# Optimization experiments

Hardware: AMD Instinct MI355X
Metric: run time of the kernel (lower is better)

Reference implementation:

```python
import jax, jax.numpy as jnp
from jax import lax
import numpy as np

B, T = 256, 512
CHAR_SIZE, CHAR_DIM, HIDDEN = 10000, 50, 256
HALF = HIDDEN // 2  # per-direction hidden size


def _lstm_dir(x, Wih, Whh, bih, bhh, reverse):
    # x: [B,T,D]; Wih: [4H,D]; Whh: [4H,H]; gate order i,f,g,o (PyTorch)
    Bsz = x.shape[0]
    H = Whh.shape[1]
    xg = jnp.einsum('btd,gd->btg', x, Wih) + bih + bhh  # precompute input gates [B,T,4H]
    def step(carry, gt):
        h, c = carry
        g = gt + h @ Whh.T
        i, f, gg, o = jnp.split(g, 4, axis=-1)
        c = jax.nn.sigmoid(f) * c + jax.nn.sigmoid(i) * jnp.tanh(gg)
        h = jax.nn.sigmoid(o) * jnp.tanh(c)
        return (h, c), h
    init = (jnp.zeros((Bsz, H), x.dtype), jnp.zeros((Bsz, H), x.dtype))
    _, hs = lax.scan(step, init, jnp.swapaxes(xg, 0, 1), reverse=reverse)
    return jnp.swapaxes(hs, 0, 1)  # [B,T,H]


def setup_inputs() -> dict:
    key = jax.random.key(0)
    ks = jax.random.split(key, 10)
    scale = np.sqrt(3.0 / CHAR_DIM)
    inp = {
        'user_text_idx': jax.random.randint(ks[0], (B, T), 0, CHAR_SIZE),
        'masks': jnp.ones((B, T), jnp.float32),
        'emb': jax.random.uniform(ks[1], (CHAR_SIZE, CHAR_DIM), jnp.float32, -scale, scale),
        'Wih_f': jax.random.normal(ks[2], (4 * HALF, CHAR_DIM), jnp.float32) * 0.08,
        'Whh_f': jax.random.normal(ks[3], (4 * HALF, HALF), jnp.float32) * 0.08,
        'bih_f': jnp.zeros((4 * HALF,), jnp.float32),
        'bhh_f': jnp.zeros((4 * HALF,), jnp.float32),
        'Wih_b': jax.random.normal(ks[4], (4 * HALF, CHAR_DIM), jnp.float32) * 0.08,
        'Whh_b': jax.random.normal(ks[5], (4 * HALF, HALF), jnp.float32) * 0.08,
        'bih_b': jnp.zeros((4 * HALF,), jnp.float32),
        'bhh_b': jnp.zeros((4 * HALF,), jnp.float32),
    }
    return inp


def reference(user_text_idx, masks, emb, Wih_f, Whh_f, bih_f, bhh_f, Wih_b, Whh_b, bih_b, bhh_b):
    x = emb[user_text_idx]                                  # [B,T,D] embedding lookup
    h_f = _lstm_dir(x, Wih_f, Whh_f, bih_f, bhh_f, False)   # forward direction
    h_b = _lstm_dir(x, Wih_b, Whh_b, bih_b, bhh_b, True)    # backward direction
    out = jnp.concatenate([h_f, h_b], axis=-1)              # [B,T,HIDDEN]
    out = out - (1.0 - masks[..., None]) * 1e8              # mask pad positions
    return jnp.max(out, axis=-2)                            # masked max-pool -> [B,HIDDEN]
```

## Files before the change

### kernel.cpp

```cpp
#include <hip/hip_runtime.h>
#include <hip/hip_fp16.h>


#define TT 512
#define CH 2

typedef _Float16 f16;
typedef _Float16 f16x8 __attribute__((ext_vector_type(8)));
typedef float f32x4 __attribute__((ext_vector_type(4)));
typedef unsigned int u32;
typedef unsigned short u16;

static __device__ __forceinline__ u32 packh2(float lo, float hi) {
    union { struct { f16 x, y; } h; u32 u; } cv;
    cv.h.x = (f16)lo; cv.h.y = (f16)hi;
    return cv.u;
}
static __device__ __forceinline__ float unpk_lo(u32 u) {
    union { u32 u; struct { f16 x, y; } h; } cv; cv.u = u;
    return (float)cv.h.x;
}
static __device__ __forceinline__ float unpk_hi(u32 u) {
    union { u32 u; struct { f16 x, y; } h; } cv; cv.u = u;
    return (float)cv.h.y;
}
static __device__ __forceinline__ float fexp(float x) {
    return __builtin_amdgcn_exp2f(x * 1.44269504088896341f);
}
static __device__ __forceinline__ float frcp(float x) {
    return __builtin_amdgcn_rcpf(x);
}
static __device__ __forceinline__ float sigf(float x) {
    return frcp(1.f + fexp(-x));
}
static __device__ __forceinline__ float xor8(float x) {
    union { float f; int i; } c; c.f = x;
    c.i = __builtin_amdgcn_mov_dpp(c.i, 0x128, 0xF, 0xF, false);
    return c.f;
}
static __device__ __forceinline__ float sel4(f32x4 v, int q) {
    return (q & 2) ? ((q & 1) ? v[3] : v[2]) : ((q & 1) ? v[1] : v[0]);
}

__global__ __attribute__((amdgpu_flat_work_group_size(1024, 1024),
                          amdgpu_num_vgpr(128)))
void bilstm_gsplit_kernel(const int* __restrict__ idx,
                          const float* __restrict__ masks,
                          const float* __restrict__ emb,
                          const float* __restrict__ Wih_f, const float* __restrict__ Whh_f,
                          const float* __restrict__ bih_f, const float* __restrict__ bhh_f,
                          const float* __restrict__ Wih_b, const float* __restrict__ Whh_b,
                          const float* __restrict__ bih_b, const float* __restrict__ bhh_b,
                          float* __restrict__ out)
{
    __shared__ __align__(16) unsigned char Hbuf[2][6 * 1024];
    __shared__ u16 idx16[CH * TT];
    __shared__ u32 mbits[TT];
    __shared__ u32 exch[CH * 128];

    const int tid  = threadIdx.x;
    const int lane = tid & 63;
    const int wv   = tid >> 6;
    const int half = wv >> 3;
    const int wvh  = wv & 7;
    const int l15  = lane & 15;
    const int c4   = lane >> 4;
    const int d    = blockIdx.x & 1;
    const int g    = blockIdx.x >> 1;
    const int b0   = g * CH;
    const int rev  = d;

    const int chain = l15 & 1;
    const int q     = (l15 >> 1) & 3;
    const int role  = l15 >> 3;

    const float* Wih = d ? Wih_b : Wih_f;
    const float* Whh = d ? Whh_b : Whh_f;
    const float* bih = d ? bih_b : bih_f;
    const float* bhh = d ? bhh_b : bhh_f;

    for (int i = tid; i < CH * TT; i += 1024) {
        const int m = i >> 9, t = i & 511;
        idx16[i] = (u16)idx[(b0 + m) * TT + t];
    }
    if (tid < TT) {
        u32 mb = 0;
        for (int m = 0; m < CH; ++m)
            mb |= (masks[(b0 + m) * TT + tid] != 0.f ? 1u : 0u) << m;
        mbits[tid] = mb;
    }
    for (int i = tid; i < 2 * 6 * 1024 / 4; i += 1024)
        ((u32*)Hbuf)[i] = 0u;

    const int tb0 = half * 256 + wvh * 16;
    const int tb1 = tb0 + 128;
    f16x8 w[6][2];
    f32x4 bias4[2];
#pragma unroll
    for (int tt = 0; tt < 2; ++tt) {
        const int n = (tt ? tb1 : tb0) + l15;
        {
            const int nb_ = (tt ? tb1 : tb0) + c4 * 4;
            const float4 bi = *(const float4*)(bih + nb_);
            const float4 bh = *(const float4*)(bhh + nb_);
            bias4[tt][0] = bi.x + bh.x; bias4[tt][1] = bi.y + bh.y;
            bias4[tt][2] = bi.z + bh.z; bias4[tt][3] = bi.w + bh.w;
        }
#pragma unroll
        for (int jj = 0; jj < 4; ++jj) {
            const float2 e = *(const float2*)(Wih + n * 50 + c4 * 8 + jj * 2);
            w[0][tt][2 * jj]     = (f16)e.x;
            w[0][tt][2 * jj + 1] = (f16)e.y;
        }
#pragma unroll
        for (int j = 0; j < 8; ++j) {
            const int k = 32 + c4 * 8 + j;
            float v = 0.f;
            if (k < 50) v = Wih[n * 50 + k];
            w[1][tt][j] = (f16)v;
        }
#pragma unroll
        for (int kt = 2; kt < 6; ++kt) {
            const int kh = (kt - 2) * 32 + c4 * 8;
            const float4 e0 = *(const float4*)(Whh + n * 128 + kh);
            const float4 e1 = *(const float4*)(Whh + n * 128 + kh + 4);
            w[kt][tt][0] = (f16)e0.x; w[kt][tt][1] = (f16)e0.y;
            w[kt][tt][2] = (f16)e0.z; w[kt][tt][3] = (f16)e0.w;
            w[kt][tt][4] = (f16)e1.x; w[kt][tt][5] = (f16)e1.y;
            w[kt][tt][6] = (f16)e1.z; w[kt][tt][7] = (f16)e1.w;
        }
    }

    __syncthreads();

    if (tid < 400) {
        const int pm = tid / 25, ps = tid % 25;
        const int t0  = rev ? (TT - 1) : 0;
        const int row = idx16[(pm & 1) * TT + t0];
        const float2 e = *(const float2*)(emb + row * 50 + ps * 2);
        const int k0 = 2 * ps;
        const int kt = k0 >> 5, c4k = (k0 >> 3) & 3, j = k0 & 7;
        *(u32*)(&Hbuf[0][(kt << 10) + ((c4k * 16 + pm) << 4) + (j << 1)]) =
            packh2(e.x, e.y);
    }
    __syncthreads();

    float cst = 0.f, rm = -3e38f;

    const int hd     = wvh * 16 + c4 * 4 + q;
    const int k0h    = 64 + hd;
    const int wb_kt  = k0h >> 5;
    const int wb_c4k = (k0h >> 3) & 3;
    const int wb_j   = k0h & 7;
    const int wb_off = (wb_kt << 10) + ((wb_c4k * 16 + chain) << 4) + (wb_j << 1)
                     + role * 128;
    const int ex     = chain * 128 + hd;

    const int  tid2  = tid - 512;
    const bool pfthr = (tid2 >= 0) && (tid2 < 400);
    const int  pm2   = pfthr ? (tid2 / 25) : 0;
    const int  ps2   = pfthr ? (tid2 % 25) : 0;

    for (int s = 0; s < TT; ++s) {
        const int cur = s & 1;
        const int t   = rev ? (TT - 1 - s) : s;

        float2 e;
        int pk0 = 0;
        const bool pf = pfthr && (s + 1 < TT);
        if (pf) {
            const int t1  = rev ? (TT - 2 - s) : (s + 1);
            const int row = idx16[(pm2 & 1) * TT + t1];
            e = *(const float2*)(emb + row * 50 + ps2 * 2);
            pk0 = 2 * ps2;
        }

        const unsigned char* hb = &Hbuf[cur][0];
        f32x4 a0 = bias4[0], a1 = bias4[1];
#pragma unroll
        for (int kt = 0; kt < 6; ++kt) {
            const f16x8 bf = *(const f16x8*)(hb + (kt << 10) + (lane << 4));
            a0 = __builtin_amdgcn_mfma_f32_16x16x32_f16(w[kt][0], bf, a0, 0, 0, 0);
            a1 = __builtin_amdgcn_mfma_f32_16x16x32_f16(w[kt][1], bf, a1, 0, 0, 0);
        }
        const float v0 = sel4(a0, q);
        const float v1 = sel4(a1, q);

        const bool rB = (role != 0);
        const float a_in = rB ? v1 : (half ? (v0 + v0) : v0);
        const float sraw = sigf(a_in);
        const float sval = (half && !rB) ? (2.f * sraw - 1.f) : sraw;
        const float sx   = xor8(sval);

        if (half) {
            const float tg = rB ? sx : sval;
            const float so = rB ? sval : sx;
            if (!rB) exch[ex] = packh2(tg, so);
        }
        const float si = rB ? sx : sval;
        const float sf = rB ? sval : sx;

        __syncthreads();

        unsigned char* nb = &Hbuf[cur ^ 1][0];
        if (!half) {
            const u32 ts = exch[ex];
            const float tg = unpk_lo(ts);
            const float so = unpk_hi(ts);
            const float cc = sf * cst + si * tg;
            cst = cc;
            const float th = 2.f * sigf(cc + cc) - 1.f;
            const float hh = so * th;
            const float pen = ((mbits[t] >> chain) & 1u) ? 0.f : 1e8f;
            rm = fmaxf(rm, hh - pen);
            const u32 pkv = packh2(hh, hh);
            *(u16*)(nb + wb_off)      = (u16)pkv;
            *(u16*)(nb + wb_off + 32) = (u16)pkv;
            *(u16*)(nb + wb_off + 64) = (u16)pkv;
            *(u16*)(nb + wb_off + 96) = (u16)pkv;
        } else if (pf) {
            const int kt = pk0 >> 5, c4k = (pk0 >> 3) & 3, j = pk0 & 7;
            *(u32*)(nb + (kt << 10) + ((c4k * 16 + pm2) << 4) + (j << 1)) =
                packh2(e.x, e.y);
        }
        __syncthreads();
    }

    if (!half && !(l15 >> 3)) {
        out[(b0 + chain) * 256 + d * 128 + hd] = rm;
    }
}

extern "C" void kernel_launch(void* const* d_in, const int* in_sizes, int n_in,
                              void* d_out, int out_size, void* d_ws, size_t ws_size,
                              hipStream_t stream) {
    const int*   idx   = (const int*)d_in[0];
    const float* masks = (const float*)d_in[1];
    const float* emb   = (const float*)d_in[2];
    const float* Wih_f = (const float*)d_in[3];
    const float* Whh_f = (const float*)d_in[4];
    const float* bih_f = (const float*)d_in[5];
    const float* bhh_f = (const float*)d_in[6];
    const float* Wih_b = (const float*)d_in[7];
    const float* Whh_b = (const float*)d_in[8];
    const float* bih_b = (const float*)d_in[9];
    const float* bhh_b = (const float*)d_in[10];
    float* out = (float*)d_out;

    bilstm_gsplit_kernel<<<dim3(256), dim3(1024), 0, stream>>>(
        idx, masks, emb,
        Wih_f, Whh_f, bih_f, bhh_f,
        Wih_b, Whh_b, bih_b, bhh_b,
        out);
}
```

Baseline: 436.7 us.

## Compact per-step hidden/input LDS buffer and broadcast B operand reads

Replaces the padded 6KB-per-buffer MFMA B-operand layout with a compact [chain][192] f16 vector per batch chain, so each lane reads its B fragment from a shared row indexed by chain and c4 rather than a per-lane slot. Hidden-state writeback drops from four replicated u16 stores per lane to one packed u32 store by a quarter of the lanes, using a DPP swap to pair neighbours. The embedding prefetch now uses 50 threads instead of 400. The aim is less LDS traffic and fewer store instructions on the serial recurrence path, at the cost of broadcast-style LDS reads where lanes share addresses.

```diff
diff --git a/kernel.cpp b/kernel.cpp
--- a/kernel.cpp
+++ b/kernel.cpp
@@ -38,22 +38,27 @@
     c.i = __builtin_amdgcn_mov_dpp(c.i, 0x128, 0xF, 0xF, false);
     return c.f;
 }
+static __device__ __forceinline__ float xor2(float x) {
+    union { float f; int i; } c; c.f = x;
+    c.i = __builtin_amdgcn_mov_dpp(c.i, 0x4E, 0xF, 0xF, false);
+    return c.f;
+}
 static __device__ __forceinline__ float sel4(f32x4 v, int q) {
     return (q & 2) ? ((q & 1) ? v[3] : v[2]) : ((q & 1) ? v[1] : v[0]);
 }
 
 __global__ __attribute__((amdgpu_flat_work_group_size(1024, 1024),
                           amdgpu_num_vgpr(128)))
-void bilstm_gsplit_kernel(const int* __restrict__ idx,
-                          const float* __restrict__ masks,
-                          const float* __restrict__ emb,
-                          const float* __restrict__ Wih_f, const float* __restrict__ Whh_f,
-                          const float* __restrict__ bih_f, const float* __restrict__ bhh_f,
-                          const float* __restrict__ Wih_b, const float* __restrict__ Whh_b,
-                          const float* __restrict__ bih_b, const float* __restrict__ bhh_b,
-                          float* __restrict__ out)
+void bilstm_gs_compact_kernel(const int* __restrict__ idx,
+                              const float* __restrict__ masks,
+                              const float* __restrict__ emb,
+                              const float* __restrict__ Wih_f, const float* __restrict__ Whh_f,
+                              const float* __restrict__ bih_f, const float* __restrict__ bhh_f,
+                              const float* __restrict__ Wih_b, const float* __restrict__ Whh_b,
+                              const float* __restrict__ bih_b, const float* __restrict__ bhh_b,
+                              float* __restrict__ out)
 {
-    __shared__ __align__(16) unsigned char Hbuf[2][6 * 1024];
+    __shared__ __align__(16) u16 Hc[2][CH][192];
     __shared__ u16 idx16[CH * TT];
     __shared__ u32 mbits[TT];
     __shared__ u32 exch[CH * 128];
@@ -89,8 +94,9 @@
             mb |= (masks[(b0 + m) * TT + tid] != 0.f ? 1u : 0u) << m;
         mbits[tid] = mb;
     }
-    for (int i = tid; i < 2 * 6 * 1024 / 4; i += 1024)
-        ((u32*)Hbuf)[i] = 0u;
+    if (tid < 2 * CH * 192 / 2) {
+        ((u32*)Hc)[tid] = 0u;
+    }
 
     const int tb0 = half * 256 + wvh * 16;
     const int tb1 = tb0 + 128;
@@ -133,53 +139,44 @@
 
     __syncthreads();
 
-    if (tid < 400) {
-        const int pm = tid / 25, ps = tid % 25;
+    const int  tid15 = tid - 960;
+    const bool xthr  = (tid15 >= 0) && (tid15 < 50);
+    const int  xch   = xthr ? (tid15 / 25) : 0;
+    const int  xps   = xthr ? (tid15 % 25) : 0;
+
+    if (xthr) {
         const int t0  = rev ? (TT - 1) : 0;
-        const int row = idx16[(pm & 1) * TT + t0];
-        const float2 e = *(const float2*)(emb + row * 50 + ps * 2);
-        const int k0 = 2 * ps;
-        const int kt = k0 >> 5, c4k = (k0 >> 3) & 3, j = k0 & 7;
-        *(u32*)(&Hbuf[0][(kt << 10) + ((c4k * 16 + pm) << 4) + (j << 1)]) =
+        const int row = idx16[xch * TT + t0];
+        const float2 e = *(const float2*)(emb + row * 50 + xps * 2);
+        *(u32*)((unsigned char*)&Hc[0][0][0] + xch * 384 + xps * 4) =
             packh2(e.x, e.y);
     }
     __syncthreads();
 
     float cst = 0.f, rm = -3e38f;
 
-    const int hd     = wvh * 16 + c4 * 4 + q;
-    const int k0h    = 64 + hd;
-    const int wb_kt  = k0h >> 5;
-    const int wb_c4k = (k0h >> 3) & 3;
-    const int wb_j   = k0h & 7;
-    const int wb_off = (wb_kt << 10) + ((wb_c4k * 16 + chain) << 4) + (wb_j << 1)
-                     + role * 128;
-    const int ex     = chain * 128 + hd;
-
-    const int  tid2  = tid - 512;
-    const bool pfthr = (tid2 >= 0) && (tid2 < 400);
-    const int  pm2   = pfthr ? (tid2 / 25) : 0;
-    const int  ps2   = pfthr ? (tid2 % 25) : 0;
+    const int hd = wvh * 16 + c4 * 4 + q;
+    const int ex = chain * 128 + hd;
+    const bool wbthr = (l15 == 0) | (l15 == 1) | (l15 == 4) | (l15 == 5);
 
     for (int s = 0; s < TT; ++s) {
         const int cur = s & 1;
         const int t   = rev ? (TT - 1 - s) : s;
 
         float2 e;
-        int pk0 = 0;
-        const bool pf = pfthr && (s + 1 < TT);
+        const bool pf = xthr && (s + 1 < TT);
         if (pf) {
             const int t1  = rev ? (TT - 2 - s) : (s + 1);
-            const int row = idx16[(pm2 & 1) * TT + t1];
-            e = *(const float2*)(emb + row * 50 + ps2 * 2);
-            pk0 = 2 * ps2;
-        }
-
-        const unsigned char* hb = &Hbuf[cur][0];
+            const int row = idx16[xch * TT + t1];
+            e = *(const float2*)(emb + row * 50 + xps * 2);
+        }
+
+        const unsigned char* hb =
+            (const unsigned char*)&Hc[cur][0][0] + chain * 384;
         f32x4 a0 = bias4[0], a1 = bias4[1];
 #pragma unroll
         for (int kt = 0; kt < 6; ++kt) {
-            const f16x8 bf = *(const f16x8*)(hb + (kt << 10) + (lane << 4));
+            const f16x8 bf = *(const f16x8*)(hb + kt * 64 + c4 * 16);
             a0 = __builtin_amdgcn_mfma_f32_16x16x32_f16(w[kt][0], bf, a0, 0, 0, 0);
             a1 = __builtin_amdgcn_mfma_f32_16x16x32_f16(w[kt][1], bf, a1, 0, 0, 0);
         }
@@ -193,16 +190,14 @@
         const float sx   = xor8(sval);
 
         if (half) {
-            const float tg = rB ? sx : sval;
-            const float so = rB ? sval : sx;
-            if (!rB) exch[ex] = packh2(tg, so);
+            if (!rB) exch[ex] = packh2(sval, sx);
         }
         const float si = rB ? sx : sval;
         const float sf = rB ? sval : sx;
 
         __syncthreads();
 
-        unsigned char* nb = &Hbuf[cur ^ 1][0];
+        unsigned char* nb = (unsigned char*)&Hc[cur ^ 1][0][0];
         if (!half) {
             const u32 ts = exch[ex];
             const float tg = unpk_lo(ts);
@@ -213,20 +208,17 @@
             const float hh = so * th;
             const float pen = ((mbits[t] >> chain) & 1u) ? 0.f : 1e8f;
             rm = fmaxf(rm, hh - pen);
-            const u32 pkv = packh2(hh, hh);
-            *(u16*)(nb + wb_off)      = (u16)pkv;
-            *(u16*)(nb + wb_off + 32) = (u16)pkv;
-            *(u16*)(nb + wb_off + 64) = (u16)pkv;
-            *(u16*)(nb + wb_off + 96) = (u16)pkv;
+            const float hx2 = xor2(hh);
+            if (wbthr) {
+                *(u32*)(nb + chain * 384 + 128 + hd * 2) = packh2(hh, hx2);
+            }
         } else if (pf) {
-            const int kt = pk0 >> 5, c4k = (pk0 >> 3) & 3, j = pk0 & 7;
-            *(u32*)(nb + (kt << 10) + ((c4k * 16 + pm2) << 4) + (j << 1)) =
-                packh2(e.x, e.y);
+            *(u32*)(nb + xch * 384 + xps * 4) = packh2(e.x, e.y);
         }
         __syncthreads();
     }
 
-    if (!half && !(l15 >> 3)) {
+    if (!half && role == 0) {
         out[(b0 + chain) * 256 + d * 128 + hd] = rm;
     }
 }
@@ -247,7 +239,7 @@
     const float* bhh_b = (const float*)d_in[10];
     float* out = (float*)d_out;
 
-    bilstm_gsplit_kernel<<<dim3(256), dim3(1024), 0, stream>>>(
+    bilstm_gs_compact_kernel<<<dim3(256), dim3(1024), 0, stream>>>(
         idx, masks, emb,
         Wih_f, Whh_f, bih_f, bhh_f,
         Wih_b, Whh_b, bih_b, bhh_b,
```

New measurement: 423.1 us. -3.1%, faster.
